# Kernel optimization log

Hardware: AMD Instinct MI355X
Metric: run time of the kernel (lower is better)

Reference implementation:

```python
import jax, jax.numpy as jnp
import numpy as np

B, T, E, H = 4, 2048, 1024, 16
S = E // H

def setup_inputs() -> dict:
    key = jax.random.key(0)
    ks = jax.random.split(key, 4)
    x = jax.random.normal(ks[0], (B, T, E), dtype=jnp.float32)
    Wk = jax.random.normal(ks[1], (E, E), dtype=jnp.float32) * (E ** -0.5)
    Wq = jax.random.normal(ks[2], (E, E), dtype=jnp.float32) * (E ** -0.5)
    Wo = jax.random.normal(ks[3], (E, E), dtype=jnp.float32) * (E ** -0.5)
    bo = jnp.zeros((E,), dtype=jnp.float32)
    return {"x": x, "Wk": Wk, "Wq": Wq, "Wo": Wo, "bo": bo}

def reference(x, Wk, Wq, Wo, bo):
    b, t, e = x.shape
    h, s = H, E // H
    scale = e ** (-0.25)  # original scales q and k each by e**(1/4)
    k = (x @ Wk).reshape(b, t, h, s).transpose(0, 2, 1, 3)  # bhts
    q = (x @ Wq).reshape(b, t, h, s).transpose(0, 2, 1, 3)
    # FAITHFUL to source: values use the KEYS projection (bug in original)
    v = (x @ Wk).reshape(b, t, h, s).transpose(0, 2, 1, 3)
    dot = jnp.einsum('bhqd,bhkd->bhqk', q * scale, k * scale)
    attn = jax.nn.softmax(dot, axis=-1)
    out = jnp.einsum('bhqk,bhkd->bhqd', attn, v)
    out = out.transpose(0, 2, 1, 3).reshape(b, t, e)
    return out @ Wo + bo
```

## Files before the change

### kernel.cpp

```cpp
#include <hip/hip_runtime.h>
#include <hip/hip_bf16.h>
#include <stdint.h>

static constexpr int kB = 4;
static constexpr int kT = 2048;
static constexpr int kE = 1024;
static constexpr int kH = 16;
static constexpr int kS = 64;
static constexpr int kRows = kB * kT;

typedef __attribute__((ext_vector_type(4)))  float    f32x4;
typedef __attribute__((ext_vector_type(16))) float    f32x16;
typedef __attribute__((ext_vector_type(4)))  float    float4v;
typedef __attribute__((ext_vector_type(8)))  __bf16   bf16x8;
typedef __attribute__((ext_vector_type(8)))  short    short8v;
typedef __attribute__((ext_vector_type(4)))  short    short4v;
typedef __attribute__((ext_vector_type(2)))  unsigned u32x2;
typedef __attribute__((ext_vector_type(4)))  unsigned u32x4;

typedef const __attribute__((address_space(1))) void gvoid_t;
typedef __attribute__((address_space(3))) void lvoid_t;

__device__ __forceinline__ short f2bf(float f) {
  union { float f; unsigned u; } c; c.f = f;
  unsigned r = (c.u + 0x7FFFu + ((c.u >> 16) & 1u)) >> 16;
  return (short)(r & 0xFFFFu);
}

__device__ __forceinline__ short bfc(float f) {
  union { __bf16 b; short s; } u; u.b = (__bf16)f; return u.s;
}

__device__ __forceinline__ unsigned cvt_pk(float lo, float hi) {
  unsigned r;
  asm("v_cvt_pk_bf16_f32 %0, %1, %2" : "=v"(r) : "v"(lo), "v"(hi));
  return r;
}

__device__ __forceinline__ void plane_swap(unsigned& a, unsigned& b) {
  asm("v_permlane32_swap_b32 %0, %1" : "+v"(a), "+v"(b));
}

#if __has_builtin(__builtin_amdgcn_exp2f)
__device__ __forceinline__ float fexp2(float x) { return __builtin_amdgcn_exp2f(x); }
#else
__device__ __forceinline__ float fexp2(float x) { return exp2f(x); }
#endif

__global__ __launch_bounds__(256)
void prep(const float* __restrict__ x, const float* __restrict__ Wk,
          const float* __restrict__ Wq, const float* __restrict__ Wo,
          short* __restrict__ Xb, short* __restrict__ WkqT,
          short* __restrict__ WoT) {
  const int bid = blockIdx.x;
  if (bid < 8192) {
    size_t i = ((size_t)bid * 256 + threadIdx.x) * 4;
    float4v v = *(const float4v*)(x + i);
    short4v o;
    o[0] = f2bf(v[0]); o[1] = f2bf(v[1]); o[2] = f2bf(v[2]); o[3] = f2bf(v[3]);
    *(short4v*)(Xb + i) = o;
    return;
  }
  __shared__ float tile[32][33];
  const int tb = bid - 8192;
  const int which = tb >> 10, t = tb & 1023;
  const float* W = (which == 0) ? Wk : ((which == 1) ? Wq : Wo);
  short* WT = (which == 0) ? WkqT : ((which == 1) ? (WkqT + kE * kE) : WoT);
  const int tx = threadIdx.x & 31, ty = threadIdx.x >> 5;
  const int c = (t & 31) * 32, r = (t >> 5) * 32;
  #pragma unroll
  for (int i = ty; i < 32; i += 8)
    tile[i][tx] = W[(size_t)(r + i) * kE + c + tx];
  __syncthreads();
  #pragma unroll
  for (int i = ty; i < 32; i += 8)
    WT[(size_t)(c + i) * kE + r + tx] = f2bf(tile[tx][i]);
}


__device__ __forceinline__ void kq_stageA(
    const short* __restrict__ gA, short* nA, int wid, int sl, int sc7) {
  #pragma unroll
  for (int h = 0; h < 2; ++h)
    #pragma unroll
    for (int i = 0; i < 2; ++i) {
      const int slot = wid * 2 + i;
      const int row = slot * 8 + sl;
      const int sc = sc7 ^ (row & 7);
      __builtin_amdgcn_global_load_lds(
          (gvoid_t*)(gA + (size_t)(h * 128 + row) * kE + 8 * sc),
          (lvoid_t*)(nA + h * 8192 + slot * 512), 16, 0, 0);
    }
}

__device__ __forceinline__ void kq_tile(
    const short* __restrict__ gA, const short* __restrict__ gB,
    const short* cA, const short* cB, short* nA, short* nB,
    bool stage, f32x4 (&acc)[8][4],
    int wid, int wm, int wn, int g, int lr, int sl, int sc7) {
  const int swz = lr & 7;
  const short* cAw = cA + wm * 8192;
  const short* cBw = cB + (wn >> 1) * 8192;
  const int brow0 = (wn & 1) * 64;
  bf16x8 af[4][2], b0[2][2], b1[2][2];

  #pragma unroll
  for (int mf = 0; mf < 4; ++mf)
    #pragma unroll
    for (int kk = 0; kk < 2; ++kk)
      af[mf][kk] = *(const bf16x8*)(cAw + (mf * 16 + lr) * 64 + (((4 * kk + g) ^ swz) << 3));
  #pragma unroll
  for (int nf = 0; nf < 2; ++nf)
    #pragma unroll
    for (int kk = 0; kk < 2; ++kk)
      b0[nf][kk] = *(const bf16x8*)(cBw + (brow0 + nf * 16 + lr) * 64 + (((4 * kk + g) ^ swz) << 3));
  if (stage) kq_stageA(gA, nA, wid, sl, sc7);
  asm volatile("" ::: "memory");
  __builtin_amdgcn_s_barrier();
  asm volatile("s_waitcnt lgkmcnt(0)" ::: "memory");
  __builtin_amdgcn_sched_barrier(0);
  __builtin_amdgcn_s_setprio(1);
  #pragma unroll
  for (int mf = 0; mf < 4; ++mf)
    #pragma unroll
    for (int nf = 0; nf < 2; ++nf)
      #pragma unroll
      for (int kk = 0; kk < 2; ++kk)
        acc[mf][nf] = __builtin_amdgcn_mfma_f32_16x16x32_bf16(af[mf][kk], b0[nf][kk], acc[mf][nf], 0, 0, 0);
  __builtin_amdgcn_s_setprio(0);
  asm volatile("" ::: "memory");
  __builtin_amdgcn_s_barrier();

  #pragma unroll
  for (int nf = 0; nf < 2; ++nf)
    #pragma unroll
    for (int kk = 0; kk < 2; ++kk)
      b1[nf][kk] = *(const bf16x8*)(cBw + (brow0 + 32 + nf * 16 + lr) * 64 + (((4 * kk + g) ^ swz) << 3));
  if (stage) kq_stageA(gB, nB, wid, sl, sc7);
  asm volatile("" ::: "memory");
  __builtin_amdgcn_s_barrier();
  asm volatile("s_waitcnt lgkmcnt(0)" ::: "memory");
  __builtin_amdgcn_sched_barrier(0);
  __builtin_amdgcn_s_setprio(1);
  #pragma unroll
  for (int mf = 0; mf < 4; ++mf)
    #pragma unroll
    for (int nf = 0; nf < 2; ++nf)
      #pragma unroll
      for (int kk = 0; kk < 2; ++kk)
        acc[mf][2 + nf] = __builtin_amdgcn_mfma_f32_16x16x32_bf16(af[mf][kk], b1[nf][kk], acc[mf][2 + nf], 0, 0, 0);
  __builtin_amdgcn_s_setprio(0);
  asm volatile("" ::: "memory");
  __builtin_amdgcn_s_barrier();

  #pragma unroll
  for (int mf = 0; mf < 4; ++mf)
    #pragma unroll
    for (int kk = 0; kk < 2; ++kk)
      af[mf][kk] = *(const bf16x8*)(cAw + (64 + mf * 16 + lr) * 64 + (((4 * kk + g) ^ swz) << 3));
  asm volatile("" ::: "memory");
  __builtin_amdgcn_s_barrier();
  asm volatile("s_waitcnt lgkmcnt(0)" ::: "memory");
  __builtin_amdgcn_sched_barrier(0);
  __builtin_amdgcn_s_setprio(1);
  #pragma unroll
  for (int mf = 0; mf < 4; ++mf)
    #pragma unroll
    for (int nf = 0; nf < 2; ++nf)
      #pragma unroll
      for (int kk = 0; kk < 2; ++kk)
        acc[4 + mf][2 + nf] = __builtin_amdgcn_mfma_f32_16x16x32_bf16(af[mf][kk], b1[nf][kk], acc[4 + mf][2 + nf], 0, 0, 0);
  __builtin_amdgcn_s_setprio(0);
  asm volatile("" ::: "memory");
  __builtin_amdgcn_s_barrier();

  #pragma unroll
  for (int nf = 0; nf < 2; ++nf)
    #pragma unroll
    for (int kk = 0; kk < 2; ++kk)
      b0[nf][kk] = *(const bf16x8*)(cBw + (brow0 + nf * 16 + lr) * 64 + (((4 * kk + g) ^ swz) << 3));
  asm volatile("s_waitcnt vmcnt(0)" ::: "memory");
  asm volatile("" ::: "memory");
  __builtin_amdgcn_s_barrier();
  asm volatile("s_waitcnt lgkmcnt(0)" ::: "memory");
  __builtin_amdgcn_sched_barrier(0);
  __builtin_amdgcn_s_setprio(1);
  #pragma unroll
  for (int mf = 0; mf < 4; ++mf)
    #pragma unroll
    for (int nf = 0; nf < 2; ++nf)
      #pragma unroll
      for (int kk = 0; kk < 2; ++kk)
        acc[4 + mf][nf] = __builtin_amdgcn_mfma_f32_16x16x32_bf16(af[mf][kk], b0[nf][kk], acc[4 + mf][nf], 0, 0, 0);
  __builtin_amdgcn_s_setprio(0);
  asm volatile("" ::: "memory");
  __builtin_amdgcn_s_barrier();
}

__global__ __launch_bounds__(512)
void gemm_kq8(const short* __restrict__ A, const short* __restrict__ BT,
              short* __restrict__ Kb, short* __restrict__ Qb,
              short* __restrict__ KT, float qs) {
  __shared__ short LA[2][16384];
  __shared__ short LB[2][16384];

  const int tid = threadIdx.x;
  const int wid = tid >> 6, lane = tid & 63;
  const int g = lane >> 4, lr = lane & 15;
  const int wm = wid >> 2, wn = wid & 3;
  const int sl = lane >> 3, sc7 = lane & 7;
  const int bid = blockIdx.x;
  const int id = (bid & 7) * 32 + (bid >> 3);
  const int n0 = (id & 7) * 256, m0 = (id >> 3) * 256;

  const short* Abase = A + (size_t)m0 * kE;
  const short* Bbase = BT + (size_t)n0 * kE;

  f32x4 acc[8][4];
  #pragma unroll
  for (int mf = 0; mf < 8; ++mf)
    #pragma unroll
    for (int nf = 0; nf < 4; ++nf)
      #pragma unroll
      for (int r = 0; r < 4; ++r) acc[mf][nf][r] = 0.f;

  kq_stageA(Abase, &LA[0][0], wid, sl, sc7);
  kq_stageA(Bbase, &LB[0][0], wid, sl, sc7);
  asm volatile("s_waitcnt vmcnt(0)" ::: "memory");
  __syncthreads();

  for (int ktp = 0; ktp < 8; ++ktp) {
    kq_tile(Abase + (2 * ktp + 1) * 64, Bbase + (2 * ktp + 1) * 64,
            &LA[0][0], &LB[0][0], &LA[1][0], &LB[1][0],
            true, acc, wid, wm, wn, g, lr, sl, sc7);
    kq_tile(Abase + (2 * ktp + 2) * 64, Bbase + (2 * ktp + 2) * 64,
            &LA[1][0], &LB[1][0], &LA[0][0], &LB[0][0],
            (2 * ktp + 1) < 15, acc, wid, wm, wn, g, lr, sl, sc7);
  }

  const int isq = (n0 >= 1024);
  short* Crm = isq ? Qb : Kb;
  const float scale = isq ? qs : 1.0f;
  const int crow = m0 + wm * 128, ccol = (n0 & 1023) + wn * 64;
  #pragma unroll
  for (int mf = 0; mf < 8; ++mf)
    #pragma unroll
    for (int nf = 0; nf < 4; ++nf)
      #pragma unroll
      for (int r = 0; r < 4; ++r)
        Crm[(size_t)(crow + mf * 16 + 4 * g + r) * kE + ccol + nf * 16 + lr] =
            bfc(acc[mf][nf][r] * scale);
  if (!isq) {
    const int b = m0 >> 11, tloc = (m0 & 2047) + wm * 128;
    const int h = (n0 + wn * 64) >> 6;
    #pragma unroll
    for (int mf = 0; mf < 8; ++mf)
      #pragma unroll
      for (int nf = 0; nf < 4; ++nf) {
        u32x2 e;
        e[0] = cvt_pk(acc[mf][nf][0], acc[mf][nf][1]);
        e[1] = cvt_pk(acc[mf][nf][2], acc[mf][nf][3]);
        *(u32x2*)(KT + (size_t)((b * 16 + h) * 64 + nf * 16 + lr) * kT +
                  tloc + mf * 16 + 4 * g) = e;
      }
  }
}

__global__ __launch_bounds__(256)
void gemm_bt(const short* __restrict__ A, const short* __restrict__ BT,
             float* __restrict__ C, const float* __restrict__ bias,
             int M, int N, int K) {
  __shared__ short As[128 * 64];
  __shared__ short Bs[128 * 64];
  const int tid = threadIdx.x;
  const int w = tid >> 6, lane = tid & 63;
  const int g = lane >> 4, lr = lane & 15;
  const int bid = blockIdx.x;
  const int id = (bid & 7) * 64 + (bid >> 3);
  const int n0 = (id & 7) * 128, m0 = (id >> 3) * 128;
  const int wr = w >> 1, wc = w & 1;
  const int srow = lane >> 3, sch = lane & 7;
  const int swz = lr & 7;

  f32x4 acc[4][4];
  #pragma unroll
  for (int m = 0; m < 4; ++m)
    #pragma unroll
    for (int n = 0; n < 4; ++n)
      #pragma unroll
      for (int r = 0; r < 4; ++r) acc[m][n][r] = 0.f;

  for (int kt = 0; kt < K; kt += 64) {
    #pragma unroll
    for (int i = 0; i < 4; ++i) {
      const int slot = w * 4 + i;
      const int row = slot * 8 + srow;
      const int sc = sch ^ srow;
      __builtin_amdgcn_global_load_lds(
          (gvoid_t*)(A + (size_t)(m0 + row) * K + kt + 8 * sc),
          (lvoid_t*)(As + slot * 512), 16, 0, 0);
      __builtin_amdgcn_global_load_lds(
          (gvoid_t*)(BT + (size_t)(n0 + row) * K + kt + 8 * sc),
          (lvoid_t*)(Bs + slot * 512), 16, 0, 0);
    }
    __syncthreads();
    #pragma unroll
    for (int kk = 0; kk < 2; ++kk) {
      bf16x8 af[4], bfr[4];
      #pragma unroll
      for (int m = 0; m < 4; ++m)
        af[m] = *(const bf16x8*)(As + (wr * 64 + m * 16 + lr) * 64 + (((4 * kk + g) ^ swz) << 3));
      #pragma unroll
      for (int n = 0; n < 4; ++n)
        bfr[n] = *(const bf16x8*)(Bs + (wc * 64 + n * 16 + lr) * 64 + (((4 * kk + g) ^ swz) << 3));
      __builtin_amdgcn_s_setprio(1);
      #pragma unroll
      for (int m = 0; m < 4; ++m)
        #pragma unroll
        for (int n = 0; n < 4; ++n)
          acc[m][n] = __builtin_amdgcn_mfma_f32_16x16x32_bf16(af[m], bfr[n], acc[m][n], 0, 0, 0);
      __builtin_amdgcn_s_setprio(0);
    }
    __syncthreads();
  }

  const int crow = m0 + wr * 64, ccol = n0 + wc * 64;
  float bv[4];
  #pragma unroll
  for (int n = 0; n < 4; ++n) bv[n] = bias[ccol + n * 16 + lr];
  #pragma unroll
  for (int m = 0; m < 4; ++m)
    #pragma unroll
    for (int n = 0; n < 4; ++n)
      #pragma unroll
      for (int r = 0; r < 4; ++r)
        C[(size_t)(crow + m * 16 + 4 * g + r) * N + ccol + n * 16 + lr] =
            acc[m][n][r] + bv[n];
}

__global__ __launch_bounds__(256, 4)
void attn_kernel(const short* Qb, const short* __restrict__ Kb,
                 const short* __restrict__ KT, short* AO) {
  __shared__ short SM[16384];

  const int tid = threadIdx.x;
  const int w = tid >> 6, lane = tid & 63;
  const int l31 = lane & 31, hi = lane >> 5;
  const int swz = l31 & 7;
  const int bid = blockIdx.x;
  const int id = (bid & 7) * 128 + (bid >> 3);
  const int q0 = (id & 15) * 128;
  const int bh = id >> 4;
  const size_t base = (size_t)(bh >> 4) * kT * kE + (size_t)(bh & 15) * kS;
  const short* Kbh = Kb + base;
  const short* KTbh = KT + (size_t)bh * 64 * kT;

  const int srow_lo = lane >> 3, sch = lane & 7;

  #pragma unroll
  for (int i = 0; i < 2; ++i) {
    const int slot = w * 2 + i, row = slot * 8 + srow_lo;
    const int sc = sch ^ (row & 7);
    __builtin_amdgcn_global_load_lds(
        (gvoid_t*)(Kbh + (size_t)row * kE + 8 * sc),
        (lvoid_t*)(SM + slot * 512), 16, 0, 0);
    __builtin_amdgcn_global_load_lds(
        (gvoid_t*)(KTbh + (size_t)row * kT + 8 * sc),
        (lvoid_t*)(SM + 8192 + slot * 512), 16, 0, 0);
  }

  bf16x8 qB[4];
  #pragma unroll
  for (int ks = 0; ks < 4; ++ks)
    qB[ks] = *(const bf16x8*)(Qb + base +
        (size_t)(q0 + w * 32 + l31) * kE + ks * 16 + hi * 8);

  f32x16 oacc[2];
  #pragma unroll
  for (int r = 0; r < 16; ++r) { oacc[0][r] = 0.f; oacc[1][r] = 0.f; }
  float lsum = 0.f;

  for (int t = 0; t < 32; ++t) {
    __syncthreads();

    if (t < 31) {
      const short* kbt = Kbh + (size_t)(t + 1) * 64 * kE;
      const short* vtt = KTbh + (size_t)(t + 1) * 64;
      short* KtN = SM + ((t + 1) & 1) * 4096;
      short* VtN = SM + 8192 + ((t + 1) & 1) * 4096;
      #pragma unroll
      for (int i = 0; i < 2; ++i) {
        const int slot = w * 2 + i, row = slot * 8 + srow_lo;
        const int sc = sch ^ (row & 7);
        __builtin_amdgcn_global_load_lds(
            (gvoid_t*)(kbt + (size_t)row * kE + 8 * sc),
            (lvoid_t*)(KtN + slot * 512), 16, 0, 0);
        __builtin_amdgcn_global_load_lds(
            (gvoid_t*)(vtt + (size_t)row * kT + 8 * sc),
            (lvoid_t*)(VtN + slot * 512), 16, 0, 0);
      }
    }

    const short* KtC = SM + (t & 1) * 4096;
    const short* VtC = SM + 8192 + (t & 1) * 4096;

    f32x16 sacc[2];
    #pragma unroll
    for (int r = 0; r < 16; ++r) { sacc[0][r] = 0.f; sacc[1][r] = 0.f; }
    #pragma unroll
    for (int ks = 0; ks < 4; ++ks) {
      const int pc = ((2 * ks + hi) ^ swz) << 3;
      bf16x8 kf0 = *(const bf16x8*)(KtC + (l31)      * 64 + pc);
      bf16x8 kf1 = *(const bf16x8*)(KtC + (32 + l31) * 64 + pc);
      __builtin_amdgcn_s_setprio(1);
      sacc[0] = __builtin_amdgcn_mfma_f32_32x32x16_bf16(kf0, qB[ks], sacc[0], 0, 0, 0);
      sacc[1] = __builtin_amdgcn_mfma_f32_32x32x16_bf16(kf1, qB[ks], sacc[1], 0, 0, 0);
      __builtin_amdgcn_s_setprio(0);
    }

    union { unsigned u[4]; bf16x8 v; } pf[4];
    #pragma unroll
    for (int kvf = 0; kvf < 2; ++kvf) {
      float pe[16];
      #pragma unroll
      for (int r = 0; r < 16; ++r) {
        pe[r] = fexp2(sacc[kvf][r]);
        lsum += pe[r];
      }
      #pragma unroll
      for (int sub = 0; sub < 2; ++sub) {
        unsigned a0 = cvt_pk(pe[8 * sub + 0], pe[8 * sub + 1]);
        unsigned b0 = cvt_pk(pe[8 * sub + 4], pe[8 * sub + 5]);
        plane_swap(a0, b0);
        unsigned a1 = cvt_pk(pe[8 * sub + 2], pe[8 * sub + 3]);
        unsigned b1 = cvt_pk(pe[8 * sub + 6], pe[8 * sub + 7]);
        plane_swap(a1, b1);
        pf[2 * kvf + sub].u[0] = a0;
        pf[2 * kvf + sub].u[1] = a1;
        pf[2 * kvf + sub].u[2] = b0;
        pf[2 * kvf + sub].u[3] = b1;
      }
    }

    #pragma unroll
    for (int ks = 0; ks < 4; ++ks) {
      const int pc = ((2 * ks + hi) ^ swz) << 3;
      bf16x8 vf0 = *(const bf16x8*)(VtC + (l31)      * 64 + pc);
      bf16x8 vf1 = *(const bf16x8*)(VtC + (32 + l31) * 64 + pc);
      __builtin_amdgcn_s_setprio(1);
      oacc[0] = __builtin_amdgcn_mfma_f32_32x32x16_bf16(vf0, pf[ks].v, oacc[0], 0, 0, 0);
      oacc[1] = __builtin_amdgcn_mfma_f32_32x32x16_bf16(vf1, pf[ks].v, oacc[1], 0, 0, 0);
      __builtin_amdgcn_s_setprio(0);
    }
  }

  __syncthreads();

  const float ltot = lsum + __shfl_xor(lsum, 32);
  const float inv = 1.f / ltot;
  short* OtW = SM + w * 2176;
  #pragma unroll
  for (int sf = 0; sf < 2; ++sf)
    #pragma unroll
    for (int c = 0; c < 4; ++c) {
      u32x2 e;
      e[0] = cvt_pk(oacc[sf][4 * c + 0] * inv, oacc[sf][4 * c + 1] * inv);
      e[1] = cvt_pk(oacc[sf][4 * c + 2] * inv, oacc[sf][4 * c + 3] * inv);
      *(u32x2*)(OtW + l31 * 68 + sf * 32 + 8 * c + 4 * hi) = e;
    }
  __builtin_amdgcn_s_barrier();
  #pragma unroll
  for (int i = 0; i < 8; ++i) {
    const int row = i * 4 + (lane >> 4);
    u32x2 v = *(const u32x2*)(OtW + row * 68 + (lane & 15) * 4);
    *(u32x2*)(AO + base + (size_t)(q0 + w * 32 + row) * kE + (lane & 15) * 4) = v;
  }
}

extern "C" void kernel_launch(void* const* d_in, const int* in_sizes, int n_in,
                              void* d_out, int out_size, void* d_ws, size_t ws_size,
                              hipStream_t stream) {
  const float* x  = (const float*)d_in[0];
  const float* Wk = (const float*)d_in[1];
  const float* Wq = (const float*)d_in[2];
  const float* Wo = (const float*)d_in[3];
  const float* bo = (const float*)d_in[4];
  float* out = (float*)d_out;

  const size_t nXE = (size_t)kRows * kE;
  const size_t nW  = (size_t)kE * kE;

  short* Xb   = (short*)d_ws;
  short* Kb   = Xb   + nXE;
  short* Qb   = Kb   + nXE;
  short* WkqT = Qb   + nXE;
  short* WoT  = WkqT + 2 * nW;
  short* KTb  = (short*)d_out;
  short* AO   = Qb;

  prep<<<dim3(8192 + 3 * 1024), 256, 0, stream>>>(
      x, Wk, Wq, Wo, Xb, WkqT, WoT);

  gemm_kq8<<<dim3(256), 512, 0, stream>>>(
      Xb, WkqT, Kb, Qb, KTb, 0.03125f * 1.44269504f);

  attn_kernel<<<dim3(1024), 256, 0, stream>>>(Qb, Kb, KTb, AO);

  gemm_bt<<<dim3(512), 256, 0, stream>>>(
      AO, WoT, out, bo, kRows, kE, kE);
}
```

Measured before the change: 162.0 us.

## Rewrite output projection GEMM as 8-wave double-buffered pipelined kernel

Replaces the simple 128x128 output-projection GEMM, which issues a global-to-LDS load and then syncs every k-step, with a 512-thread kernel that uses 256x128 tiles and double-buffered LDS. The kernel prefetches the next k-tile while MFMAs run, split into four phases with barriers and setprio. It reuses the staging scheme of the fused K/Q GEMM. The goal is to hide global load latency and to reuse each B tile across more rows. The cost is a grid of 256 blocks, which may underfill the CUs, and many barriers per k-step.

```diff
diff --git a/kernel.cpp b/kernel.cpp
--- a/kernel.cpp
+++ b/kernel.cpp
@@ -93,6 +93,19 @@
     }
 }
 
+__device__ __forceinline__ void bt_stageB(
+    const short* __restrict__ gB, short* nB, int wid, int sl, int sc7) {
+  #pragma unroll
+  for (int i = 0; i < 2; ++i) {
+    const int slot = wid * 2 + i;
+    const int row = slot * 8 + sl;
+    const int sc = sc7 ^ (row & 7);
+    __builtin_amdgcn_global_load_lds(
+        (gvoid_t*)(gB + (size_t)row * kE + 8 * sc),
+        (lvoid_t*)(nB + slot * 512), 16, 0, 0);
+  }
+}
+
 __device__ __forceinline__ void kq_tile(
     const short* __restrict__ gA, const short* __restrict__ gB,
     const short* cA, const short* cB, short* nA, short* nB,
@@ -266,76 +279,153 @@
   }
 }
 
-__global__ __launch_bounds__(256)
-void gemm_bt(const short* __restrict__ A, const short* __restrict__ BT,
-             float* __restrict__ C, const float* __restrict__ bias,
-             int M, int N, int K) {
-  __shared__ short As[128 * 64];
-  __shared__ short Bs[128 * 64];
+__global__ __launch_bounds__(512)
+void gemm_bt8(const short* __restrict__ A, const short* __restrict__ BT,
+              float* __restrict__ C, const float* __restrict__ bias) {
+  __shared__ short LA[2][16384];
+  __shared__ short LB[2][8192];
+
   const int tid = threadIdx.x;
-  const int w = tid >> 6, lane = tid & 63;
+  const int wid = tid >> 6, lane = tid & 63;
   const int g = lane >> 4, lr = lane & 15;
+  const int wm = wid >> 1, wn = wid & 1;
+  const int sl = lane >> 3, sc7 = lane & 7;
+  const int swz = lr & 7;
   const int bid = blockIdx.x;
-  const int id = (bid & 7) * 64 + (bid >> 3);
-  const int n0 = (id & 7) * 128, m0 = (id >> 3) * 128;
-  const int wr = w >> 1, wc = w & 1;
-  const int srow = lane >> 3, sch = lane & 7;
-  const int swz = lr & 7;
+  const int id = (bid & 7) * 32 + (bid >> 3);
+  const int n0 = (id & 7) * 128, m0 = (id >> 3) * 256;
+
+  const short* Abase = A + (size_t)m0 * kE;
+  const short* Bbase = BT + (size_t)n0 * kE;
 
   f32x4 acc[4][4];
   #pragma unroll
-  for (int m = 0; m < 4; ++m)
-    #pragma unroll
-    for (int n = 0; n < 4; ++n)
-      #pragma unroll
-      for (int r = 0; r < 4; ++r) acc[m][n][r] = 0.f;
-
-  for (int kt = 0; kt < K; kt += 64) {
-    #pragma unroll
-    for (int i = 0; i < 4; ++i) {
-      const int slot = w * 4 + i;
-      const int row = slot * 8 + srow;
-      const int sc = sch ^ srow;
-      __builtin_amdgcn_global_load_lds(
-          (gvoid_t*)(A + (size_t)(m0 + row) * K + kt + 8 * sc),
-          (lvoid_t*)(As + slot * 512), 16, 0, 0);
-      __builtin_amdgcn_global_load_lds(
-          (gvoid_t*)(BT + (size_t)(n0 + row) * K + kt + 8 * sc),
-          (lvoid_t*)(Bs + slot * 512), 16, 0, 0);
+  for (int mf = 0; mf < 4; ++mf)
+    #pragma unroll
+    for (int nf = 0; nf < 4; ++nf)
+      #pragma unroll
+      for (int r = 0; r < 4; ++r) acc[mf][nf][r] = 0.f;
+
+  kq_stageA(Abase, &LA[0][0], wid, sl, sc7);
+  bt_stageB(Bbase, &LB[0][0], wid, sl, sc7);
+  asm volatile("s_waitcnt vmcnt(0)" ::: "memory");
+  __syncthreads();
+
+  for (int ktp = 0; ktp < 8; ++ktp) {
+    #pragma unroll
+    for (int half = 0; half < 2; ++half) {
+      const int kt = 2 * ktp + half;
+      const short* cA = &LA[kt & 1][0];
+      const short* cB = &LB[kt & 1][0];
+      short* nA = &LA[(kt + 1) & 1][0];
+      short* nB = &LB[(kt + 1) & 1][0];
+      const bool stage = kt < 15;
+      const short* gA = Abase + (kt + 1) * 64;
+      const short* gB = Bbase + (kt + 1) * 64;
+      const short* cAw = cA + wm * 4096;
+      const short* cBw = cB + wn * 4096;
+      bf16x8 af[2][2], b0[2][2], b1[2][2];
+
+      #pragma unroll
+      for (int mf = 0; mf < 2; ++mf)
+        #pragma unroll
+        for (int kk = 0; kk < 2; ++kk)
+          af[mf][kk] = *(const bf16x8*)(cAw + (mf * 16 + lr) * 64 + (((4 * kk + g) ^ swz) << 3));
+      #pragma unroll
+      for (int nf = 0; nf < 2; ++nf)
+        #pragma unroll
+        for (int kk = 0; kk < 2; ++kk)
+          b0[nf][kk] = *(const bf16x8*)(cBw + (nf * 16 + lr) * 64 + (((4 * kk + g) ^ swz) << 3));
+      if (stage) kq_stageA(gA, nA, wid, sl, sc7);
+      asm volatile("" ::: "memory");
+      __builtin_amdgcn_s_barrier();
+      asm volatile("s_waitcnt lgkmcnt(0)" ::: "memory");
+      __builtin_amdgcn_sched_barrier(0);
+      __builtin_amdgcn_s_setprio(1);
+      #pragma unroll
+      for (int mf = 0; mf < 2; ++mf)
+        #pragma unroll
+        for (int nf = 0; nf < 2; ++nf)
+          #pragma unroll
+          for (int kk = 0; kk < 2; ++kk)
+            acc[mf][nf] = __builtin_amdgcn_mfma_f32_16x16x32_bf16(af[mf][kk], b0[nf][kk], acc[mf][nf], 0, 0, 0);
+      __builtin_amdgcn_s_setprio(0);
+      asm volatile("" ::: "memory");
+      __builtin_amdgcn_s_barrier();
+
+      #pragma unroll
+      for (int nf = 0; nf < 2; ++nf)
+        #pragma unroll
+        for (int kk = 0; kk < 2; ++kk)
+          b1[nf][kk] = *(const bf16x8*)(cBw + (32 + nf * 16 + lr) * 64 + (((4 * kk + g) ^ swz) << 3));
+      if (stage) bt_stageB(gB, nB, wid, sl, sc7);
+      asm volatile("" ::: "memory");
+      __builtin_amdgcn_s_barrier();
+      asm volatile("s_waitcnt lgkmcnt(0)" ::: "memory");
+      __builtin_amdgcn_sched_barrier(0);
+      __builtin_amdgcn_s_setprio(1);
+      #pragma unroll
+      for (int mf = 0; mf < 2; ++mf)
+        #pragma unroll
+        for (int nf = 0; nf < 2; ++nf)
+          #pragma unroll
+          for (int kk = 0; kk < 2; ++kk)
+            acc[mf][2 + nf] = __builtin_amdgcn_mfma_f32_16x16x32_bf16(af[mf][kk], b1[nf][kk], acc[mf][2 + nf], 0, 0, 0);
+      __builtin_amdgcn_s_setprio(0);
+      asm volatile("" ::: "memory");
+      __builtin_amdgcn_s_barrier();
+
+      #pragma unroll
+      for (int mf = 0; mf < 2; ++mf)
+        #pragma unroll
+        for (int kk = 0; kk < 2; ++kk)
+          af[mf][kk] = *(const bf16x8*)(cAw + (32 + mf * 16 + lr) * 64 + (((4 * kk + g) ^ swz) << 3));
+      asm volatile("" ::: "memory");
+      __builtin_amdgcn_s_barrier();
+      asm volatile("s_waitcnt lgkmcnt(0)" ::: "memory");
+      __builtin_amdgcn_sched_barrier(0);
+      __builtin_amdgcn_s_setprio(1);
+      #pragma unroll
+      for (int mf = 0; mf < 2; ++mf)
+        #pragma unroll
+        for (int nf = 0; nf < 2; ++nf)
+          #pragma unroll
+          for (int kk = 0; kk < 2; ++kk)
+            acc[2 + mf][2 + nf] = __builtin_amdgcn_mfma_f32_16x16x32_bf16(af[mf][kk], b1[nf][kk], acc[2 + mf][2 + nf], 0, 0, 0);
+      __builtin_amdgcn_s_setprio(0);
+      asm volatile("" ::: "memory");
+      __builtin_amdgcn_s_barrier();
+
+      asm volatile("s_waitcnt vmcnt(0)" ::: "memory");
+      asm volatile("" ::: "memory");
+      __builtin_amdgcn_s_barrier();
+      __builtin_amdgcn_sched_barrier(0);
+      __builtin_amdgcn_s_setprio(1);
+      #pragma unroll
+      for (int mf = 0; mf < 2; ++mf)
+        #pragma unroll
+        for (int nf = 0; nf < 2; ++nf)
+          #pragma unroll
+          for (int kk = 0; kk < 2; ++kk)
+            acc[2 + mf][nf] = __builtin_amdgcn_mfma_f32_16x16x32_bf16(af[mf][kk], b0[nf][kk], acc[2 + mf][nf], 0, 0, 0);
+      __builtin_amdgcn_s_setprio(0);
+      asm volatile("" ::: "memory");
+      __builtin_amdgcn_s_barrier();
     }
-    __syncthreads();
-    #pragma unroll
-    for (int kk = 0; kk < 2; ++kk) {
-      bf16x8 af[4], bfr[4];
-      #pragma unroll
-      for (int m = 0; m < 4; ++m)
-        af[m] = *(const bf16x8*)(As + (wr * 64 + m * 16 + lr) * 64 + (((4 * kk + g) ^ swz) << 3));
-      #pragma unroll
-      for (int n = 0; n < 4; ++n)
-        bfr[n] = *(const bf16x8*)(Bs + (wc * 64 + n * 16 + lr) * 64 + (((4 * kk + g) ^ swz) << 3));
-      __builtin_amdgcn_s_setprio(1);
-      #pragma unroll
-      for (int m = 0; m < 4; ++m)
-        #pragma unroll
-        for (int n = 0; n < 4; ++n)
-          acc[m][n] = __builtin_amdgcn_mfma_f32_16x16x32_bf16(af[m], bfr[n], acc[m][n], 0, 0, 0);
-      __builtin_amdgcn_s_setprio(0);
-    }
-    __syncthreads();
-  }
-
-  const int crow = m0 + wr * 64, ccol = n0 + wc * 64;
+  }
+
+  const int crow = m0 + wm * 64, ccol = n0 + wn * 64;
   float bv[4];
   #pragma unroll
-  for (int n = 0; n < 4; ++n) bv[n] = bias[ccol + n * 16 + lr];
-  #pragma unroll
-  for (int m = 0; m < 4; ++m)
-    #pragma unroll
-    for (int n = 0; n < 4; ++n)
+  for (int nf = 0; nf < 4; ++nf) bv[nf] = bias[ccol + nf * 16 + lr];
+  #pragma unroll
+  for (int mf = 0; mf < 4; ++mf)
+    #pragma unroll
+    for (int nf = 0; nf < 4; ++nf)
       #pragma unroll
       for (int r = 0; r < 4; ++r)
-        C[(size_t)(crow + m * 16 + 4 * g + r) * N + ccol + n * 16 + lr] =
-            acc[m][n][r] + bv[n];
+        C[(size_t)(crow + mf * 16 + 4 * g + r) * kE + ccol + nf * 16 + lr] =
+            acc[mf][nf][r] + bv[nf];
 }
 
 __global__ __launch_bounds__(256, 4)
@@ -506,6 +596,5 @@
 
   attn_kernel<<<dim3(1024), 256, 0, stream>>>(Qb, Kb, KTb, AO);
 
-  gemm_bt<<<dim3(512), 256, 0, stream>>>(
-      AO, WoT, out, bo, kRows, kE, kE);
-}
+  gemm_bt8<<<dim3(256), 512, 0, stream>>>(AO, WoT, out, bo);
+}
```

New measurement: 160.7 us, median of 2. Within noise of the previous version (-0.8%).
